# Optimization experiments

Measured on AMD Instinct MI355X. Metric: run time of the kernel, lower is better.

The kernel has to match this reference:

```python
import jax, jax.numpy as jnp
import numpy as np

B, L, V, D, H, DK, NL, M = 4, 1024, 64, 256, 4, 64, 4, 20
FF = 4 * D
EPS = 1e-5


def _rel_table(seq_len, m):
    # abs(i-j), log-bucketed beyond m, clipped to [0, 2m] -> int indices [L, L]
    d = jnp.abs(jnp.arange(seq_len)[:, None] - jnp.arange(seq_len)[None, :]).astype(jnp.float32)
    d = jnp.where(d > m, m + jnp.log2(jnp.maximum(d - m, 1.0)), d)
    return jnp.clip(d, 0, 2 * m).astype(jnp.int32)


def _layer_norm(x, g, b):
    mu = jnp.mean(x, axis=-1, keepdims=True)
    var = jnp.mean(jnp.square(x - mu), axis=-1, keepdims=True)
    return (x - mu) * jax.lax.rsqrt(var + EPS) * g + b


def setup_inputs() -> dict:
    key = jax.random.key(0)
    ks = jax.random.split(key, 16)
    w = lambda i, shape: jax.random.normal(ks[i], shape, jnp.float32) * 0.05
    return {
        "x": jax.random.normal(ks[0], (B, L, V), jnp.float32),
        "emb": w(1, (V, D)),
        "Wq": w(2, (NL, D, H * DK)), "bq": jnp.zeros((NL, H * DK), jnp.float32),
        "Wk": w(3, (NL, D, H * DK)), "bk": jnp.zeros((NL, H * DK), jnp.float32),
        "Wv": w(4, (NL, D, H * DK)), "bv": jnp.zeros((NL, H * DK), jnp.float32),
        "Wo": w(5, (NL, H * DK, D)), "bo": jnp.zeros((NL, D), jnp.float32),
        "rel_k": 1.0 + w(6, (NL, 2 * M + 1, H)),  # multiplicative bias ~1
        "rel_b": w(7, (NL, 2 * M + 1, H)),
        "ln1_g": jnp.ones((NL, D), jnp.float32), "ln1_b": jnp.zeros((NL, D), jnp.float32),
        "W1": w(8, (NL, D, FF)), "b1": jnp.zeros((NL, FF), jnp.float32),
        "W2": w(9, (NL, FF, D)), "b2": jnp.zeros((NL, D), jnp.float32),
        "ln2_g": jnp.ones((NL, D), jnp.float32), "ln2_b": jnp.zeros((NL, D), jnp.float32),
    }


def reference(x, emb, Wq, bq, Wk, bk, Wv, bv, Wo, bo, rel_k, rel_b,
              ln1_g, ln1_b, W1, b1, W2, b2, ln2_g, ln2_b):
    h = x @ emb  # [B, L, D]  (dropout inactive: eval mode)
    table = _rel_table(L, M)  # [L, L] int32
    inv_sqrt_dk = jnp.float32(1.0 / np.sqrt(DK))
    attns = []
    for l in range(NL):
        q = (h @ Wq[l] + bq[l]).reshape(B, L, H, DK)
        k = (h @ Wk[l] + bk[l]).reshape(B, L, H, DK)
        v = (h @ Wv[l] + bv[l]).reshape(B, L, H, DK)
        scores = jnp.einsum('blhk,bmhk->bhlm', q, k) * inv_sqrt_dk
        # per-head relative-position bias (table symmetric, so axis order of L,L is immaterial)
        bias_k = jnp.transpose(rel_k[l][table], (2, 1, 0))  # [H, L, L]
        bias_b = jnp.transpose(rel_b[l][table], (2, 1, 0))  # [H, L, L]
        scores = scores * bias_k[None] + bias_b[None]
        attn = jax.nn.softmax(scores, axis=-1)  # attn dropout inactive (eval)
        attns.append(attn)
        out = jnp.einsum('bhlm,bmhk->blhk', attn, v).reshape(B, L, H * DK) @ Wo[l] + bo[l]
        # FeedForwardNetwork (note: source has NO residual connections)
        y = _layer_norm(out, ln1_g[l], ln1_b[l])
        y = jax.nn.gelu(y @ W1[l] + b1[l], approximate=False) @ W2[l] + b2[l]
        h = _layer_norm(y, ln2_g[l], ln2_b[l])
    avg_attn = jnp.mean(jnp.stack(attns, axis=0), axis=0)  # [B, H, L, L]
    return h.mean(axis=1), avg_attn
```

## Files before the change

kernel.cpp:

```cpp
#include <hip/hip_runtime.h>
#include <hip/hip_bf16.h>
#include <math.h>

#define Bn 4
#define Ln 1024
#define Vn 64
#define Dn 256
#define Hn 4
#define DKn 64
#define NLn 4
#define Mn 20
#define FFn 1024
#define NTOK (Bn * Ln)
#define QKVW 768
#define LOG2E 1.4426950408889634f
#define PELEMS (Bn * Hn * Ln * Ln)

typedef __attribute__((ext_vector_type(8))) short bf16x8;
typedef __attribute__((ext_vector_type(4))) float f32x4;

__device__ __forceinline__ ushort f2b(float f) {
    uint u = __float_as_uint(f);
    u += 0x7fff + ((u >> 16) & 1);
    return (ushort)(u >> 16);
}
__device__ __forceinline__ float b2f(ushort u) {
    return __uint_as_float(((uint)u) << 16);
}

__global__ __launch_bounds__(256) void embed_k(const float* __restrict__ X,
                                               const float* __restrict__ E,
                                               ushort* __restrict__ Hb) {
    __shared__ float xs[Vn];
    int n = blockIdx.x, d = threadIdx.x;
    if (threadIdx.x < Vn) xs[threadIdx.x] = X[n * Vn + threadIdx.x];
    __syncthreads();
    float s = 0.f;
#pragma unroll
    for (int v = 0; v < Vn; ++v) s += xs[v] * E[v * Dn + d];
    Hb[(size_t)n * Dn + d] = f2b(s);
}

__global__ __launch_bounds__(256) void relbias_k(const float* __restrict__ rk,
                                                 const float* __restrict__ rb,
                                                 float* __restrict__ bkT,
                                                 float* __restrict__ bbT) {
    int tid = blockIdx.x * 256 + threadIdx.x;
    int dist = tid & 1023;
    int hh = (tid >> 10) & 3;
    int l = tid >> 12;
    float dd = (float)dist;
    if (dist > Mn) dd = (float)Mn + log2f((float)(dist - Mn));
    if (dd > 2.0f * Mn) dd = 2.0f * Mn;
    int idx = (int)dd;
    bkT[tid] = rk[(l * (2 * Mn + 1) + idx) * Hn + hh] * 0.125f * LOG2E;
    bbT[tid] = rb[(l * (2 * Mn + 1) + idx) * Hn + hh] * LOG2E;
}

__global__ __launch_bounds__(256) void prep_bias(const float* __restrict__ bq,
                                                 const float* __restrict__ bk,
                                                 const float* __restrict__ bv,
                                                 float* __restrict__ bqkv) {
    int idx = blockIdx.x * 256 + threadIdx.x;
    int l = idx / QKVW, r = idx - l * QKVW;
    float v;
    if (r < 256)      v = bq[l * 256 + r];
    else if (r < 512) v = bk[l * 256 + r - 256];
    else              v = bv[l * 256 + r - 512];
    bqkv[idx] = v;
}

__global__ __launch_bounds__(256) void transpose_cvt(
    const float* __restrict__ src, ushort* __restrict__ dst,
    int R, int C, int srcLS, int dstLS) {
    __shared__ float s[32][33];
    src += (size_t)blockIdx.z * srcLS;
    dst += (size_t)blockIdx.z * dstLS;
    int r0 = blockIdx.y * 32, c0 = blockIdx.x * 32;
    int tx = threadIdx.x & 31, ty = threadIdx.x >> 5;
#pragma unroll
    for (int ii = 0; ii < 4; ++ii)
        s[ty + 8 * ii][tx] = src[(size_t)(r0 + ty + 8 * ii) * C + c0 + tx];
    __syncthreads();
#pragma unroll
    for (int ii = 0; ii < 4; ++ii)
        dst[(size_t)(c0 + ty + 8 * ii) * R + r0 + tx] = f2b(s[tx][ty + 8 * ii]);
}

__global__ __launch_bounds__(256) void transpose_v(const ushort* __restrict__ qkv,
                                                   ushort* __restrict__ Vt) {
    __shared__ ushort s[32][65];
    int j0 = blockIdx.x * 32;
    int bh = blockIdx.y;
    int b = bh >> 2, hh = bh & 3;
    int t = threadIdx.x;
#pragma unroll
    for (int ii = 0; ii < 8; ++ii) {
        int e = t + 256 * ii;
        int jr = e >> 6, dc = e & 63;
        s[jr][dc] = qkv[(size_t)(b * Ln + j0 + jr) * QKVW + 2 * Dn + hh * DKn + dc];
    }
    __syncthreads();
#pragma unroll
    for (int ii = 0; ii < 8; ++ii) {
        int e = t + 256 * ii;
        int dr = e >> 5, jc = e & 31;
        Vt[(size_t)(bh * DKn + dr) * Ln + j0 + jc] = s[jc][dr];
    }
}

#define GST 40
__global__ __launch_bounds__(256) void gemm_mfma(
    const ushort* __restrict__ A, const ushort* __restrict__ Bt,
    const float* __restrict__ bias, ushort* __restrict__ C,
    int M, int N, int K, int act) {
    __shared__ __align__(16) ushort As[64 * GST];
    __shared__ __align__(16) ushort Bs[64 * GST];
    int t = threadIdx.x;
    int lane = t & 63, w = t >> 6;
    int wm = w >> 1, wn = w & 1;
    int l15 = lane & 15, lg = lane >> 4;
    int mBase = blockIdx.y * 64, nBase = blockIdx.x * 64;
    int lrow = t >> 2, lkc = (t & 3) * 8;
    const ushort* Ap = A + (size_t)(mBase + lrow) * K + lkc;
    const ushort* Bp = Bt + (size_t)(nBase + lrow) * K + lkc;
    f32x4 acc[2][2] = {};
    for (int k0 = 0; k0 < K; k0 += 32) {
        uint4 av = *(const uint4*)(Ap + k0);
        uint4 bv = *(const uint4*)(Bp + k0);
        __syncthreads();
        *(uint4*)&As[lrow * GST + lkc] = av;
        *(uint4*)&Bs[lrow * GST + lkc] = bv;
        __syncthreads();
        bf16x8 a0 = *(const bf16x8*)&As[(wm * 32 + l15) * GST + lg * 8];
        bf16x8 a1 = *(const bf16x8*)&As[(wm * 32 + 16 + l15) * GST + lg * 8];
        bf16x8 b0 = *(const bf16x8*)&Bs[(wn * 32 + l15) * GST + lg * 8];
        bf16x8 b1 = *(const bf16x8*)&Bs[(wn * 32 + 16 + l15) * GST + lg * 8];
        acc[0][0] = __builtin_amdgcn_mfma_f32_16x16x32_bf16(a0, b0, acc[0][0], 0, 0, 0);
        acc[0][1] = __builtin_amdgcn_mfma_f32_16x16x32_bf16(a0, b1, acc[0][1], 0, 0, 0);
        acc[1][0] = __builtin_amdgcn_mfma_f32_16x16x32_bf16(a1, b0, acc[1][0], 0, 0, 0);
        acc[1][1] = __builtin_amdgcn_mfma_f32_16x16x32_bf16(a1, b1, acc[1][1], 0, 0, 0);
    }
#pragma unroll
    for (int ni = 0; ni < 2; ++ni) {
        int col = nBase + wn * 32 + ni * 16 + l15;
        float bc = bias[col];
#pragma unroll
        for (int mi = 0; mi < 2; ++mi) {
            int rb = mBase + wm * 32 + mi * 16 + lg * 4;
#pragma unroll
            for (int j = 0; j < 4; ++j) {
                float v = acc[mi][ni][j] + bc;
                if (act) v = v * 0.5f * (1.0f + erff(v * 0.7071067811865475f));
                C[(size_t)(rb + j) * N + col] = f2b(v);
            }
        }
    }
}

#define PWST 40
template <int MODE>
__global__ __launch_bounds__(256) void attn_fused(
    const ushort* __restrict__ qkv, const ushort* __restrict__ Vt,
    const float* __restrict__ bkTab, const float* __restrict__ bbTab,
    ushort* __restrict__ ctx, float* __restrict__ avg,
    ushort* __restrict__ Pout, int first) {
    __shared__ float bk_l[Ln];
    __shared__ float bb_l[Ln];
    __shared__ __align__(16) ushort Pw[4][2][16 * PWST];
    __shared__ float mm[4][16];
    __shared__ float ll[4][16];
    __shared__ float Opart[4][1024];

    int t = threadIdx.x;
    int lane = t & 63, wn = t >> 6;
    int l15 = lane & 15, lg = lane >> 4;

    int bid = blockIdx.x;
    int xcd = bid & 7, sub = bid >> 3;
    int bh = xcd * 2 + (sub >> 6);
    int q = sub & 63;
    int b = bh >> 2, hh = bh & 3;
    int i0 = q * 16;

#pragma unroll
    for (int ii = 0; ii < 4; ++ii) {
        bk_l[t + 256 * ii] = bkTab[hh * Ln + t + 256 * ii];
        bb_l[t + 256 * ii] = bbTab[hh * Ln + t + 256 * ii];
    }
    __syncthreads();

    bf16x8 qa0, qa1;
    {
        const ushort* qp = qkv + (size_t)(b * Ln + i0 + l15) * QKVW + hh * DKn;
        qa0 = *(const bf16x8*)(qp + lg * 8);
        qa1 = *(const bf16x8*)(qp + 32 + lg * 8);
    }

    const ushort* kbase = qkv + (size_t)(b * Ln) * QKVW + Dn + hh * DKn;

    f32x4 sv[16];
    float m[4] = {-1e30f, -1e30f, -1e30f, -1e30f};
#pragma unroll
    for (int c = 0; c < 16; ++c) {
        const ushort* kp = kbase + (size_t)(c * 64 + wn * 16 + l15) * QKVW;
        bf16x8 k0 = *(const bf16x8*)(kp + lg * 8);
        bf16x8 k1 = *(const bf16x8*)(kp + 32 + lg * 8);
        f32x4 acc = {};
        acc = __builtin_amdgcn_mfma_f32_16x16x32_bf16(qa0, k0, acc, 0, 0, 0);
        acc = __builtin_amdgcn_mfma_f32_16x16x32_bf16(qa1, k1, acc, 0, 0, 0);
        int j = c * 64 + wn * 16 + l15;
#pragma unroll
        for (int r = 0; r < 4; ++r) {
            int i = i0 + lg * 4 + r;
            int dist = (i > j) ? (i - j) : (j - i);
            float s = acc[r] * bk_l[dist] + bb_l[dist];
            sv[c][r] = s;
            m[r] = fmaxf(m[r], s);
        }
    }
#pragma unroll
    for (int mask = 1; mask < 16; mask <<= 1)
#pragma unroll
        for (int r = 0; r < 4; ++r) m[r] = fmaxf(m[r], __shfl_xor(m[r], mask, 64));
    if (l15 == 0)
#pragma unroll
        for (int r = 0; r < 4; ++r) mm[wn][lg * 4 + r] = m[r];
    __syncthreads();
#pragma unroll
    for (int r = 0; r < 4; ++r) {
        int row = lg * 4 + r;
        m[r] = fmaxf(fmaxf(mm[0][row], mm[1][row]), fmaxf(mm[2][row], mm[3][row]));
    }
    float lsum[4] = {0.f, 0.f, 0.f, 0.f};
#pragma unroll
    for (int c = 0; c < 16; ++c)
#pragma unroll
        for (int r = 0; r < 4; ++r) {
            float p = exp2f(sv[c][r] - m[r]);
            sv[c][r] = p;
            lsum[r] += p;
        }
#pragma unroll
    for (int mask = 1; mask < 16; mask <<= 1)
#pragma unroll
        for (int r = 0; r < 4; ++r) lsum[r] += __shfl_xor(lsum[r], mask, 64);
    if (l15 == 0)
#pragma unroll
        for (int r = 0; r < 4; ++r) ll[wn][lg * 4 + r] = lsum[r];
    __syncthreads();
    float invl[4];
#pragma unroll
    for (int r = 0; r < 4; ++r) {
        int row = lg * 4 + r;
        invl[r] = 1.0f / (ll[0][row] + ll[1][row] + ll[2][row] + ll[3][row]);
    }

    const ushort* vbase = Vt + (size_t)bh * DKn * Ln;
    float* avgrow = avg + ((size_t)bh * Ln + i0) * Ln;
    ushort* prow = Pout + ((size_t)bh * Ln + i0) * Ln;
    int iw = lane >> 2, jq = lane & 3;
    f32x4 acco[4] = {};
#pragma unroll
    for (int p = 0; p < 8; ++p) {
        const int c0 = 2 * p, c1 = 2 * p + 1;
        float aold[2][4];
        if (MODE == 0 && !first) {
#pragma unroll
            for (int cc = 0; cc < 2; ++cc)
#pragma unroll
                for (int r = 0; r < 4; ++r)
                    aold[cc][r] = avgrow[(size_t)(lg * 4 + r) * Ln +
                                         (c0 + cc) * 64 + wn * 16 + l15];
        }
        float pn[2][4];
#pragma unroll
        for (int cc = 0; cc < 2; ++cc)
#pragma unroll
            for (int r = 0; r < 4; ++r) {
                float pv = sv[c0 + cc][r] * invl[r];
                pn[cc][r] = pv;
                ushort ph = f2b(pv);
                int off = (lg * 4 + r) * PWST + cc * 16 + l15;
                Pw[wn][0][off] = ph;
                Pw[wn][1][off] = f2b(pv - b2f(ph));
            }
        int kcol = (lg < 2 ? c0 : c1) * 64 + wn * 16 + (lg & 1) * 8;
        bf16x8 va0 = *(const bf16x8*)(vbase + (size_t)(0 * 16 + l15) * Ln + kcol);
        bf16x8 va1 = *(const bf16x8*)(vbase + (size_t)(1 * 16 + l15) * Ln + kcol);
        bf16x8 va2 = *(const bf16x8*)(vbase + (size_t)(2 * 16 + l15) * Ln + kcol);
        bf16x8 va3 = *(const bf16x8*)(vbase + (size_t)(3 * 16 + l15) * Ln + kcol);
        bf16x8 pbh = *(const bf16x8*)&Pw[wn][0][l15 * PWST + lg * 8];
        bf16x8 pbl = *(const bf16x8*)&Pw[wn][1][l15 * PWST + lg * 8];
        acco[0] = __builtin_amdgcn_mfma_f32_16x16x32_bf16(va0, pbh, acco[0], 0, 0, 0);
        acco[1] = __builtin_amdgcn_mfma_f32_16x16x32_bf16(va1, pbh, acco[1], 0, 0, 0);
        acco[2] = __builtin_amdgcn_mfma_f32_16x16x32_bf16(va2, pbh, acco[2], 0, 0, 0);
        acco[3] = __builtin_amdgcn_mfma_f32_16x16x32_bf16(va3, pbh, acco[3], 0, 0, 0);
        acco[0] = __builtin_amdgcn_mfma_f32_16x16x32_bf16(va0, pbl, acco[0], 0, 0, 0);
        acco[1] = __builtin_amdgcn_mfma_f32_16x16x32_bf16(va1, pbl, acco[1], 0, 0, 0);
        acco[2] = __builtin_amdgcn_mfma_f32_16x16x32_bf16(va2, pbl, acco[2], 0, 0, 0);
        acco[3] = __builtin_amdgcn_mfma_f32_16x16x32_bf16(va3, pbl, acco[3], 0, 0, 0);
        if (MODE == 0) {
#pragma unroll
            for (int cc = 0; cc < 2; ++cc)
#pragma unroll
                for (int r = 0; r < 4; ++r) {
                    float v = 0.25f * pn[cc][r];
                    if (!first) v += aold[cc][r];
                    avgrow[(size_t)(lg * 4 + r) * Ln + (c0 + cc) * 64 + wn * 16 + l15] = v;
                }
        } else {
            ushort4 ph0 = *(const ushort4*)&Pw[wn][0][iw * PWST + 0 * 16 + jq * 4];
            ushort4 ph1 = *(const ushort4*)&Pw[wn][0][iw * PWST + 1 * 16 + jq * 4];
            *(ushort4*)&prow[(size_t)iw * Ln + c0 * 64 + wn * 16 + jq * 4] = ph0;
            *(ushort4*)&prow[(size_t)iw * Ln + c1 * 64 + wn * 16 + jq * 4] = ph1;
        }
    }

#pragma unroll
    for (int dg = 0; dg < 4; ++dg)
#pragma unroll
        for (int r = 0; r < 4; ++r)
            Opart[wn][(dg * 16 + lg * 4 + r) * 16 + l15] = acco[dg][r];
    __syncthreads();
#pragma unroll
    for (int k = 0; k < 4; ++k) {
        int idx = t + 256 * k;
        float v = Opart[0][idx] + Opart[1][idx] + Opart[2][idx] + Opart[3][idx];
        int dd = idx >> 4, ii = idx & 15;
        ctx[(size_t)(b * Ln + i0 + ii) * Dn + hh * DKn + dd] = f2b(v);
    }
}

__global__ __launch_bounds__(256) void avg_sum_k(const ushort* __restrict__ P,
                                                 float* __restrict__ avg) {
    size_t e = ((size_t)blockIdx.x * 256 + threadIdx.x) * 4;
    ushort4 a = *(const ushort4*)&P[e];
    ushort4 b4 = *(const ushort4*)&P[(size_t)PELEMS + e];
    ushort4 c4 = *(const ushort4*)&P[(size_t)2 * PELEMS + e];
    ushort4 d4 = *(const ushort4*)&P[(size_t)3 * PELEMS + e];
    float4 o;
    o.x = 0.25f * (b2f(a.x) + b2f(b4.x) + b2f(c4.x) + b2f(d4.x));
    o.y = 0.25f * (b2f(a.y) + b2f(b4.y) + b2f(c4.y) + b2f(d4.y));
    o.z = 0.25f * (b2f(a.z) + b2f(b4.z) + b2f(c4.z) + b2f(d4.z));
    o.w = 0.25f * (b2f(a.w) + b2f(b4.w) + b2f(c4.w) + b2f(d4.w));
    *(float4*)&avg[e] = o;
}

__global__ __launch_bounds__(256) void layernorm_k(const ushort* __restrict__ X,
                                                   const float* __restrict__ g,
                                                   const float* __restrict__ bta,
                                                   ushort* __restrict__ Y) {
    int w = threadIdx.x >> 6, lane = threadIdx.x & 63;
    int row = blockIdx.x * 4 + w;
    const ushort* xr = X + (size_t)row * Dn;
    float x[4];
#pragma unroll
    for (int ii = 0; ii < 4; ++ii) x[ii] = b2f(xr[lane + 64 * ii]);
    float s = x[0] + x[1] + x[2] + x[3];
#pragma unroll
    for (int m = 1; m < 64; m <<= 1) s += __shfl_xor(s, m, 64);
    float mu = s * (1.0f / 256.0f);
    float vs = 0.f;
#pragma unroll
    for (int ii = 0; ii < 4; ++ii) {
        float d = x[ii] - mu;
        vs += d * d;
    }
#pragma unroll
    for (int m = 1; m < 64; m <<= 1) vs += __shfl_xor(vs, m, 64);
    float rs = rsqrtf(vs * (1.0f / 256.0f) + 1e-5f);
#pragma unroll
    for (int ii = 0; ii < 4; ++ii) {
        int d = lane + 64 * ii;
        Y[(size_t)row * Dn + d] = f2b((x[ii] - mu) * rs * g[d] + bta[d]);
    }
}

__global__ __launch_bounds__(256) void mean_part_k(const ushort* __restrict__ Hb,
                                                   float* __restrict__ part) {
    int blk = blockIdx.x;
    int b = blk >> 4, g = blk & 15;
    int d = threadIdx.x;
    float s = 0.f;
#pragma unroll
    for (int r = 0; r < 64; ++r)
        s += b2f(Hb[(size_t)(b * Ln + g * 64 + r) * Dn + d]);
    part[(size_t)blk * Dn + d] = s;
}
__global__ __launch_bounds__(256) void mean_final_k(const float* __restrict__ part,
                                                    float* __restrict__ out) {
    int b = blockIdx.x, d = threadIdx.x;
    float s = 0.f;
#pragma unroll
    for (int g = 0; g < 16; ++g) s += part[(size_t)(b * 16 + g) * Dn + d];
    out[b * Dn + d] = s * (1.0f / (float)Ln);
}

extern "C" void kernel_launch(void* const* d_in, const int* in_sizes, int n_in,
                              void* d_out, int out_size, void* d_ws, size_t ws_size,
                              hipStream_t stream) {
    const float* x    = (const float*)d_in[0];
    const float* emb  = (const float*)d_in[1];
    const float* Wq   = (const float*)d_in[2];
    const float* bq   = (const float*)d_in[3];
    const float* Wk   = (const float*)d_in[4];
    const float* bk   = (const float*)d_in[5];
    const float* Wv   = (const float*)d_in[6];
    const float* bv   = (const float*)d_in[7];
    const float* Wo   = (const float*)d_in[8];
    const float* bo   = (const float*)d_in[9];
    const float* rk   = (const float*)d_in[10];
    const float* rb   = (const float*)d_in[11];
    const float* ln1g = (const float*)d_in[12];
    const float* ln1b = (const float*)d_in[13];
    const float* W1   = (const float*)d_in[14];
    const float* b1   = (const float*)d_in[15];
    const float* W2   = (const float*)d_in[16];
    const float* b2   = (const float*)d_in[17];
    const float* ln2g = (const float*)d_in[18];
    const float* ln2b = (const float*)d_in[19];

    float* out = (float*)d_out;
    float* avg = out + Bn * Dn;

    char* ws = (char*)d_ws;
    const size_t MB = 1024 * 1024;
    ushort* hb   = (ushort*)(ws);
    ushort* qkvb = (ushort*)(ws + 2 * MB);
    ushort* ctxb = (ushort*)(ws + 8 * MB);
    ushort* t1   = (ushort*)(ws + 10 * MB);
    ushort* ffb  = (ushort*)(ws + 12 * MB);
    ushort* qkvT = (ushort*)(ws + 20 * MB);
    ushort* WoT  = (ushort*)(ws + 22 * MB);
    ushort* W1T  = (ushort*)(ws + 23 * MB);
    ushort* W2T  = (ushort*)(ws + 25 * MB);
    float*  bqkv = (float*)(ws + 27 * MB);
    float*  bkT  = (float*)(ws + 27 * MB + 65536);
    float*  bbT  = (float*)(ws + 27 * MB + 131072);
    ushort* Vt   = (ushort*)(ws + 30 * MB);
    float*  mpart= (float*)(ws + 33 * MB);
    ushort* Pbuf = (ushort*)(ws + 36 * MB);

    const size_t need = 36 * MB + (size_t)4 * PELEMS * sizeof(ushort);
    const bool fancy = (ws_size >= need);

    embed_k<<<NTOK, 256, 0, stream>>>(x, emb, hb);
    relbias_k<<<64, 256, 0, stream>>>(rk, rb, bkT, bbT);
    prep_bias<<<12, 256, 0, stream>>>(bq, bk, bv, bqkv);

    dim3 t88(8, 8, NLn);
    transpose_cvt<<<t88, 256, 0, stream>>>(Wq, qkvT + 0,      256, 256, 65536, 196608);
    transpose_cvt<<<t88, 256, 0, stream>>>(Wk, qkvT + 65536,  256, 256, 65536, 196608);
    transpose_cvt<<<t88, 256, 0, stream>>>(Wv, qkvT + 131072, 256, 256, 65536, 196608);
    transpose_cvt<<<t88, 256, 0, stream>>>(Wo, WoT,           256, 256, 65536, 65536);
    transpose_cvt<<<dim3(32, 8, NLn), 256, 0, stream>>>(W1, W1T, 256, 1024, 262144, 262144);
    transpose_cvt<<<dim3(8, 32, NLn), 256, 0, stream>>>(W2, W2T, 1024, 256, 262144, 262144);

    for (int l = 0; l < NLn; ++l) {
        gemm_mfma<<<dim3(12, 64), 256, 0, stream>>>(
            hb, qkvT + (size_t)l * 196608, bqkv + l * QKVW, qkvb, NTOK, QKVW, Dn, 0);
        transpose_v<<<dim3(32, 16), 256, 0, stream>>>(qkvb, Vt);
        if (fancy) {
            attn_fused<1><<<1024, 256, 0, stream>>>(
                qkvb, Vt, bkT + l * Hn * Ln, bbT + l * Hn * Ln, ctxb, avg,
                Pbuf + (size_t)l * PELEMS, (l == 0) ? 1 : 0);
        } else {
            attn_fused<0><<<1024, 256, 0, stream>>>(
                qkvb, Vt, bkT + l * Hn * Ln, bbT + l * Hn * Ln, ctxb, avg,
                (ushort*)Pbuf, (l == 0) ? 1 : 0);
        }
        gemm_mfma<<<dim3(4, 64), 256, 0, stream>>>(
            ctxb, WoT + (size_t)l * 65536, bo + l * 256, t1, NTOK, Dn, Dn, 0);
        layernorm_k<<<NTOK / 4, 256, 0, stream>>>(
            t1, ln1g + l * 256, ln1b + l * 256, t1);
        gemm_mfma<<<dim3(16, 64), 256, 0, stream>>>(
            t1, W1T + (size_t)l * 262144, b1 + l * FFn, ffb, NTOK, FFn, Dn, 1);
        gemm_mfma<<<dim3(4, 64), 256, 0, stream>>>(
            ffb, W2T + (size_t)l * 262144, b2 + l * 256, hb, NTOK, Dn, FFn, 0);
        layernorm_k<<<NTOK / 4, 256, 0, stream>>>(
            hb, ln2g + l * 256, ln2b + l * 256, hb);
    }
    if (fancy) {
        avg_sum_k<<<PELEMS / (256 * 4), 256, 0, stream>>>(Pbuf, avg);
    }
    mean_part_k<<<64, 256, 0, stream>>>(hb, mpart);
    mean_final_k<<<Bn, 256, 0, stream>>>(mpart, out);
}
```

Baseline: 426.4 us.

## Split attention key range across 8 waves and widen avg_sum vector loads

The fused attention kernel now runs 512 threads per block (8 waves), and the two wave groups each cover half of the key columns. This halves per-thread score registers and loop length, and the row max, row sum and output partials are reduced across 8 waves through shared memory. The goal is more latency hiding and lower register pressure per wave, at the cost of more shared memory for Opart and larger cross-wave reductions. Separately, avg_sum_k processes 8 elements per thread with 16-byte loads, halving its grid.

```diff
diff --git a/kernel.cpp b/kernel.cpp
--- a/kernel.cpp
+++ b/kernel.cpp
@@ -159,21 +159,23 @@
 }
 
 #define PWST 40
+#define NW 8
 template <int MODE>
-__global__ __launch_bounds__(256) void attn_fused(
+__global__ __launch_bounds__(512) void attn_fused(
     const ushort* __restrict__ qkv, const ushort* __restrict__ Vt,
     const float* __restrict__ bkTab, const float* __restrict__ bbTab,
     ushort* __restrict__ ctx, float* __restrict__ avg,
     ushort* __restrict__ Pout, int first) {
     __shared__ float bk_l[Ln];
     __shared__ float bb_l[Ln];
-    __shared__ __align__(16) ushort Pw[4][2][16 * PWST];
-    __shared__ float mm[4][16];
-    __shared__ float ll[4][16];
-    __shared__ float Opart[4][1024];
+    __shared__ __align__(16) ushort Pw[NW][2][16 * PWST];
+    __shared__ float mm[NW][16];
+    __shared__ float ll[NW][16];
+    __shared__ float Opart[NW][1024];
 
     int t = threadIdx.x;
-    int lane = t & 63, wn = t >> 6;
+    int lane = t & 63, w = t >> 6;
+    int wn = w & 3, wc = w >> 2;
     int l15 = lane & 15, lg = lane >> 4;
 
     int bid = blockIdx.x;
@@ -184,9 +186,9 @@
     int i0 = q * 16;
 
 #pragma unroll
-    for (int ii = 0; ii < 4; ++ii) {
-        bk_l[t + 256 * ii] = bkTab[hh * Ln + t + 256 * ii];
-        bb_l[t + 256 * ii] = bbTab[hh * Ln + t + 256 * ii];
+    for (int ii = 0; ii < 2; ++ii) {
+        bk_l[t + 512 * ii] = bkTab[hh * Ln + t + 512 * ii];
+        bb_l[t + 512 * ii] = bbTab[hh * Ln + t + 512 * ii];
     }
     __syncthreads();
 
@@ -199,10 +201,11 @@
 
     const ushort* kbase = qkv + (size_t)(b * Ln) * QKVW + Dn + hh * DKn;
 
-    f32x4 sv[16];
+    f32x4 sv[8];
     float m[4] = {-1e30f, -1e30f, -1e30f, -1e30f};
 #pragma unroll
-    for (int c = 0; c < 16; ++c) {
+    for (int cl = 0; cl < 8; ++cl) {
+        int c = wc * 8 + cl;
         const ushort* kp = kbase + (size_t)(c * 64 + wn * 16 + l15) * QKVW;
         bf16x8 k0 = *(const bf16x8*)(kp + lg * 8);
         bf16x8 k1 = *(const bf16x8*)(kp + 32 + lg * 8);
@@ -215,7 +218,7 @@
             int i = i0 + lg * 4 + r;
             int dist = (i > j) ? (i - j) : (j - i);
             float s = acc[r] * bk_l[dist] + bb_l[dist];
-            sv[c][r] = s;
+            sv[cl][r] = s;
             m[r] = fmaxf(m[r], s);
         }
     }
@@ -225,20 +228,22 @@
         for (int r = 0; r < 4; ++r) m[r] = fmaxf(m[r], __shfl_xor(m[r], mask, 64));
     if (l15 == 0)
 #pragma unroll
-        for (int r = 0; r < 4; ++r) mm[wn][lg * 4 + r] = m[r];
+        for (int r = 0; r < 4; ++r) mm[w][lg * 4 + r] = m[r];
     __syncthreads();
 #pragma unroll
     for (int r = 0; r < 4; ++r) {
         int row = lg * 4 + r;
-        m[r] = fmaxf(fmaxf(mm[0][row], mm[1][row]), fmaxf(mm[2][row], mm[3][row]));
+        float m0 = fmaxf(fmaxf(mm[0][row], mm[1][row]), fmaxf(mm[2][row], mm[3][row]));
+        float m1 = fmaxf(fmaxf(mm[4][row], mm[5][row]), fmaxf(mm[6][row], mm[7][row]));
+        m[r] = fmaxf(m0, m1);
     }
     float lsum[4] = {0.f, 0.f, 0.f, 0.f};
 #pragma unroll
-    for (int c = 0; c < 16; ++c)
+    for (int cl = 0; cl < 8; ++cl)
 #pragma unroll
         for (int r = 0; r < 4; ++r) {
-            float p = exp2f(sv[c][r] - m[r]);
-            sv[c][r] = p;
+            float p = exp2f(sv[cl][r] - m[r]);
+            sv[cl][r] = p;
             lsum[r] += p;
         }
 #pragma unroll
@@ -247,13 +252,14 @@
         for (int r = 0; r < 4; ++r) lsum[r] += __shfl_xor(lsum[r], mask, 64);
     if (l15 == 0)
 #pragma unroll
-        for (int r = 0; r < 4; ++r) ll[wn][lg * 4 + r] = lsum[r];
+        for (int r = 0; r < 4; ++r) ll[w][lg * 4 + r] = lsum[r];
     __syncthreads();
     float invl[4];
 #pragma unroll
     for (int r = 0; r < 4; ++r) {
         int row = lg * 4 + r;
-        invl[r] = 1.0f / (ll[0][row] + ll[1][row] + ll[2][row] + ll[3][row]);
+        invl[r] = 1.0f / (ll[0][row] + ll[1][row] + ll[2][row] + ll[3][row] +
+                          ll[4][row] + ll[5][row] + ll[6][row] + ll[7][row]);
     }
 
     const ushort* vbase = Vt + (size_t)bh * DKn * Ln;
@@ -262,8 +268,8 @@
     int iw = lane >> 2, jq = lane & 3;
     f32x4 acco[4] = {};
 #pragma unroll
-    for (int p = 0; p < 8; ++p) {
-        const int c0 = 2 * p, c1 = 2 * p + 1;
+    for (int p = 0; p < 4; ++p) {
+        const int c0 = wc * 8 + 2 * p, c1 = c0 + 1;
         float aold[2][4];
         if (MODE == 0 && !first) {
 #pragma unroll
@@ -273,25 +279,24 @@
                     aold[cc][r] = avgrow[(size_t)(lg * 4 + r) * Ln +
                                          (c0 + cc) * 64 + wn * 16 + l15];
         }
-        float pn[2][4];
 #pragma unroll
         for (int cc = 0; cc < 2; ++cc)
 #pragma unroll
             for (int r = 0; r < 4; ++r) {
-                float pv = sv[c0 + cc][r] * invl[r];
-                pn[cc][r] = pv;
+                float pv = sv[2 * p + cc][r] * invl[r];
+                sv[2 * p + cc][r] = pv;
                 ushort ph = f2b(pv);
                 int off = (lg * 4 + r) * PWST + cc * 16 + l15;
-                Pw[wn][0][off] = ph;
-                Pw[wn][1][off] = f2b(pv - b2f(ph));
+                Pw[w][0][off] = ph;
+                Pw[w][1][off] = f2b(pv - b2f(ph));
             }
         int kcol = (lg < 2 ? c0 : c1) * 64 + wn * 16 + (lg & 1) * 8;
         bf16x8 va0 = *(const bf16x8*)(vbase + (size_t)(0 * 16 + l15) * Ln + kcol);
         bf16x8 va1 = *(const bf16x8*)(vbase + (size_t)(1 * 16 + l15) * Ln + kcol);
         bf16x8 va2 = *(const bf16x8*)(vbase + (size_t)(2 * 16 + l15) * Ln + kcol);
         bf16x8 va3 = *(const bf16x8*)(vbase + (size_t)(3 * 16 + l15) * Ln + kcol);
-        bf16x8 pbh = *(const bf16x8*)&Pw[wn][0][l15 * PWST + lg * 8];
-        bf16x8 pbl = *(const bf16x8*)&Pw[wn][1][l15 * PWST + lg * 8];
+        bf16x8 pbh = *(const bf16x8*)&Pw[w][0][l15 * PWST + lg * 8];
+        bf16x8 pbl = *(const bf16x8*)&Pw[w][1][l15 * PWST + lg * 8];
         acco[0] = __builtin_amdgcn_mfma_f32_16x16x32_bf16(va0, pbh, acco[0], 0, 0, 0);
         acco[1] = __builtin_amdgcn_mfma_f32_16x16x32_bf16(va1, pbh, acco[1], 0, 0, 0);
         acco[2] = __builtin_amdgcn_mfma_f32_16x16x32_bf16(va2, pbh, acco[2], 0, 0, 0);
@@ -305,13 +310,13 @@
             for (int cc = 0; cc < 2; ++cc)
 #pragma unroll
                 for (int r = 0; r < 4; ++r) {
-                    float v = 0.25f * pn[cc][r];
+                    float v = 0.25f * sv[2 * p + cc][r];
                     if (!first) v += aold[cc][r];
                     avgrow[(size_t)(lg * 4 + r) * Ln + (c0 + cc) * 64 + wn * 16 + l15] = v;
                 }
         } else {
-            ushort4 ph0 = *(const ushort4*)&Pw[wn][0][iw * PWST + 0 * 16 + jq * 4];
-            ushort4 ph1 = *(const ushort4*)&Pw[wn][0][iw * PWST + 1 * 16 + jq * 4];
+            ushort4 ph0 = *(const ushort4*)&Pw[w][0][iw * PWST + 0 * 16 + jq * 4];
+            ushort4 ph1 = *(const ushort4*)&Pw[w][0][iw * PWST + 1 * 16 + jq * 4];
             *(ushort4*)&prow[(size_t)iw * Ln + c0 * 64 + wn * 16 + jq * 4] = ph0;
             *(ushort4*)&prow[(size_t)iw * Ln + c1 * 64 + wn * 16 + jq * 4] = ph1;
         }
@@ -321,12 +326,13 @@
     for (int dg = 0; dg < 4; ++dg)
 #pragma unroll
         for (int r = 0; r < 4; ++r)
-            Opart[wn][(dg * 16 + lg * 4 + r) * 16 + l15] = acco[dg][r];
-    __syncthreads();
-#pragma unroll
-    for (int k = 0; k < 4; ++k) {
-        int idx = t + 256 * k;
-        float v = Opart[0][idx] + Opart[1][idx] + Opart[2][idx] + Opart[3][idx];
+            Opart[w][(dg * 16 + lg * 4 + r) * 16 + l15] = acco[dg][r];
+    __syncthreads();
+#pragma unroll
+    for (int k = 0; k < 2; ++k) {
+        int idx = t + 512 * k;
+        float v = Opart[0][idx] + Opart[1][idx] + Opart[2][idx] + Opart[3][idx] +
+                  Opart[4][idx] + Opart[5][idx] + Opart[6][idx] + Opart[7][idx];
         int dd = idx >> 4, ii = idx & 15;
         ctx[(size_t)(b * Ln + i0 + ii) * Dn + hh * DKn + dd] = f2b(v);
     }
@@ -334,17 +340,26 @@
 
 __global__ __launch_bounds__(256) void avg_sum_k(const ushort* __restrict__ P,
                                                  float* __restrict__ avg) {
-    size_t e = ((size_t)blockIdx.x * 256 + threadIdx.x) * 4;
-    ushort4 a = *(const ushort4*)&P[e];
-    ushort4 b4 = *(const ushort4*)&P[(size_t)PELEMS + e];
-    ushort4 c4 = *(const ushort4*)&P[(size_t)2 * PELEMS + e];
-    ushort4 d4 = *(const ushort4*)&P[(size_t)3 * PELEMS + e];
-    float4 o;
-    o.x = 0.25f * (b2f(a.x) + b2f(b4.x) + b2f(c4.x) + b2f(d4.x));
-    o.y = 0.25f * (b2f(a.y) + b2f(b4.y) + b2f(c4.y) + b2f(d4.y));
-    o.z = 0.25f * (b2f(a.z) + b2f(b4.z) + b2f(c4.z) + b2f(d4.z));
-    o.w = 0.25f * (b2f(a.w) + b2f(b4.w) + b2f(c4.w) + b2f(d4.w));
-    *(float4*)&avg[e] = o;
+    size_t e = ((size_t)blockIdx.x * 256 + threadIdx.x) * 8;
+    uint4 a = *(const uint4*)&P[e];
+    uint4 b4 = *(const uint4*)&P[(size_t)PELEMS + e];
+    uint4 c4 = *(const uint4*)&P[(size_t)2 * PELEMS + e];
+    uint4 d4 = *(const uint4*)&P[(size_t)3 * PELEMS + e];
+    const ushort* ap = (const ushort*)&a;
+    const ushort* bp = (const ushort*)&b4;
+    const ushort* cp = (const ushort*)&c4;
+    const ushort* dp = (const ushort*)&d4;
+    float4 o0, o1;
+    float* o0p = (float*)&o0;
+    float* o1p = (float*)&o1;
+#pragma unroll
+    for (int k = 0; k < 4; ++k)
+        o0p[k] = 0.25f * (b2f(ap[k]) + b2f(bp[k]) + b2f(cp[k]) + b2f(dp[k]));
+#pragma unroll
+    for (int k = 0; k < 4; ++k)
+        o1p[k] = 0.25f * (b2f(ap[4 + k]) + b2f(bp[4 + k]) + b2f(cp[4 + k]) + b2f(dp[4 + k]));
+    *(float4*)&avg[e] = o0;
+    *(float4*)&avg[e + 4] = o1;
 }
 
 __global__ __launch_bounds__(256) void layernorm_k(const ushort* __restrict__ X,
@@ -462,11 +477,11 @@
             hb, qkvT + (size_t)l * 196608, bqkv + l * QKVW, qkvb, NTOK, QKVW, Dn, 0);
         transpose_v<<<dim3(32, 16), 256, 0, stream>>>(qkvb, Vt);
         if (fancy) {
-            attn_fused<1><<<1024, 256, 0, stream>>>(
+            attn_fused<1><<<1024, 512, 0, stream>>>(
                 qkvb, Vt, bkT + l * Hn * Ln, bbT + l * Hn * Ln, ctxb, avg,
                 Pbuf + (size_t)l * PELEMS, (l == 0) ? 1 : 0);
         } else {
-            attn_fused<0><<<1024, 256, 0, stream>>>(
+            attn_fused<0><<<1024, 512, 0, stream>>>(
                 qkvb, Vt, bkT + l * Hn * Ln, bbT + l * Hn * Ln, ctxb, avg,
                 (ushort*)Pbuf, (l == 0) ? 1 : 0);
         }
@@ -482,7 +497,7 @@
             hb, ln2g + l * 256, ln2b + l * 256, hb);
     }
     if (fancy) {
-        avg_sum_k<<<PELEMS / (256 * 4), 256, 0, stream>>>(Pbuf, avg);
+        avg_sum_k<<<PELEMS / (256 * 8), 256, 0, stream>>>(Pbuf, avg);
     }
     mean_part_k<<<64, 256, 0, stream>>>(hb, mpart);
     mean_final_k<<<Bn, 256, 0, stream>>>(mpart, out);
```

New measurement: 419.3 us. About the same (-1.7%).
